# Kernel optimization log

Measured on AMD Instinct MI355X. Metric: run time of the kernel, lower is better.

The kernel has to match this reference:

```python
import jax, jax.numpy as jnp
import numpy as np

BATCH, L, OUT, DIM, VOCAB, K = 25, 11, 4, 2048, 32000, 1024


def setup_inputs() -> dict:
    key = jax.random.key(0)
    k1, k2, k3 = jax.random.split(key, 3)
    h = jax.random.normal(k1, (BATCH, L, OUT, DIM), dtype=jnp.float32)
    lm_head_weight = jax.random.normal(k2, (VOCAB, DIM), dtype=jnp.float32) * 0.02
    index = jax.random.randint(k3, (BATCH, L, K), 0, VOCAB, dtype=jnp.int64)
    return {"h": h, "lm_head_weight": lm_head_weight, "index": index}


def reference(h, lm_head_weight, index):
    # Faithful to torch: full-vocab matmul h @ weight.T, then gather selected ids.
    # h: (b, l, o, d); weight: (v, d) -> logits: (b, l, o, v)
    logits = jnp.einsum('blod,vd->blov', h, lm_head_weight)
    # gather along vocab dim with index (b, l, k) expanded over the o axis
    b, l, o, v = logits.shape
    idx = jnp.broadcast_to(index[:, :, None, :], (b, l, o, index.shape[-1]))
    result = jnp.take_along_axis(logits, idx, axis=3)  # (b, l, o, k)
    return result
```

## Files before the change

kernel.cpp:

```cpp
#include <hip/hip_runtime.h>

#define BATCH 25
#define LSEQ  11
#define OUTR  4
#define DIM   2048
#define VOCAB 32000
#define KSEL  1024

typedef _Float16 half8  __attribute__((ext_vector_type(8)));
typedef float    floatx4 __attribute__((ext_vector_type(4)));

#define WH_BYTES ((size_t)VOCAB * DIM * 2)

__global__ __launch_bounds__(256) void conv_f16(const float* __restrict__ w,
                                                _Float16* __restrict__ wh) {
    const size_t i = ((size_t)blockIdx.x * 256 + threadIdx.x) * 8;
    const floatx4 a = __builtin_nontemporal_load((const floatx4*)(w + i));
    const floatx4 b = __builtin_nontemporal_load((const floatx4*)(w + i + 4));
    half8 hv;
    hv[0] = (_Float16)a[0]; hv[1] = (_Float16)a[1];
    hv[2] = (_Float16)a[2]; hv[3] = (_Float16)a[3];
    hv[4] = (_Float16)b[0]; hv[5] = (_Float16)b[1];
    hv[6] = (_Float16)b[2]; hv[7] = (_Float16)b[3];
    *(half8*)(wh + i) = hv;
}

#define TPW 4
#define KPB (4 * TPW * 16)
#define NKC (KSEL / KPB)
#define ROWE 2080

__global__ __launch_bounds__(256) void gather_mfma(
    const float*    __restrict__ h,
    const _Float16* __restrict__ wh,
    const int*      __restrict__ index,
    float*          __restrict__ out)
{
    __shared__ _Float16 hs[OUTR * ROWE];

    const int bl   = blockIdx.x / NKC;
    const int kc   = blockIdx.x % NKC;
    const int tid  = threadIdx.x;
    const int wave = tid >> 6;
    const int lane = tid & 63;
    const int quad = lane >> 4;
    const int n    = lane & 15;
    const int row  = lane & 3;

    const float* hp = h + (size_t)bl * (OUTR * DIM);
#pragma unroll
    for (int o = 0; o < OUTR; ++o) {
        const int e = o * DIM + tid * 8;
        const floatx4 a = *(const floatx4*)(hp + e);
        const floatx4 b = *(const floatx4*)(hp + e + 4);
        half8 hv;
        hv[0] = (_Float16)a[0]; hv[1] = (_Float16)a[1];
        hv[2] = (_Float16)a[2]; hv[3] = (_Float16)a[3];
        hv[4] = (_Float16)b[0]; hv[5] = (_Float16)b[1];
        hv[6] = (_Float16)b[2]; hv[7] = (_Float16)b[3];
        *(half8*)(hs + o * ROWE + tid * 8) = hv;
    }
    __syncthreads();

    const int kb_blk = kc * KPB;
    const _Float16* bptr[TPW];
#pragma unroll
    for (int t = 0; t < TPW; ++t) {
        const int k_id = kb_blk + (wave * TPW + t) * 16 + n;
        const int ridx = index[(size_t)bl * KSEL + k_id];
        bptr[t] = wh + (size_t)ridx * DIM + quad * 8;
    }

    const _Float16* aptr = hs + row * ROWE + quad * 8;

    floatx4 acc[TPW];
#pragma unroll
    for (int t = 0; t < TPW; ++t) acc[t] = (floatx4){0.f, 0.f, 0.f, 0.f};

#pragma unroll 4
    for (int ks = 0; ks < DIM / 32; ++ks) {
        const half8 a = *(const half8*)(aptr + ks * 32);
        half8 b[TPW];
#pragma unroll
        for (int t = 0; t < TPW; ++t)
            b[t] = *(const half8*)(bptr[t] + ks * 32);
#pragma unroll
        for (int t = 0; t < TPW; ++t)
            acc[t] = __builtin_amdgcn_mfma_f32_16x16x32_f16(a, b[t], acc[t], 0, 0, 0);
    }

    if (quad == 0) {
        float* op = out + (size_t)bl * (OUTR * KSEL) + kb_blk;
#pragma unroll
        for (int t = 0; t < TPW; ++t) {
            const int kcol = (wave * TPW + t) * 16 + n;
#pragma unroll
            for (int r = 0; r < OUTR; ++r)
                op[r * KSEL + kcol] = acc[t][r];
        }
    }
}

#define FKPB 64
#define FKPW 16

__global__ __launch_bounds__(256) void ehead_f32_kernel(
    const float* __restrict__ h,
    const float* __restrict__ wt,
    const int*   __restrict__ index,
    float*       __restrict__ out)
{
    const int nkc = KSEL / FKPB;
    const int bl  = blockIdx.x / nkc;
    const int kc  = blockIdx.x % nkc;
    const int kbase = kc * FKPB;

    __shared__ float hsf[OUTR * DIM];
    const float* hp = h + (size_t)bl * (OUTR * DIM);
    const int tid = threadIdx.x;
#pragma unroll
    for (int i = 0; i < (OUTR * DIM) / (256 * 4); ++i) {
        const int e = (i * 256 + tid) * 4;
        *(float4*)&hsf[e] = *(const float4*)&hp[e];
    }
    __syncthreads();

    const int wave = tid >> 6;
    const int lane = tid & 63;
    const int* ip = index + (size_t)bl * KSEL + kbase + wave * FKPW;
    float*     op = out   + (size_t)bl * (OUTR * KSEL) + kbase + wave * FKPW;

    for (int g = 0; g < FKPW; g += 4) {
        const float4* r0 = (const float4*)(wt + (size_t)ip[g + 0] * DIM);
        const float4* r1 = (const float4*)(wt + (size_t)ip[g + 1] * DIM);
        const float4* r2 = (const float4*)(wt + (size_t)ip[g + 2] * DIM);
        const float4* r3 = (const float4*)(wt + (size_t)ip[g + 3] * DIM);
        float acc[OUTR][4];
#pragma unroll
        for (int o = 0; o < OUTR; ++o)
#pragma unroll
            for (int kk = 0; kk < 4; ++kk) acc[o][kk] = 0.f;
#pragma unroll
        for (int c = 0; c < DIM / 256; ++c) {
            const int off = c * 64 + lane;
            const float4 w0 = r0[off];
            const float4 w1 = r1[off];
            const float4 w2 = r2[off];
            const float4 w3 = r3[off];
#pragma unroll
            for (int o = 0; o < OUTR; ++o) {
                const float4 hv = *(const float4*)&hsf[o * DIM + off * 4];
                acc[o][0] += hv.x * w0.x + hv.y * w0.y + hv.z * w0.z + hv.w * w0.w;
                acc[o][1] += hv.x * w1.x + hv.y * w1.y + hv.z * w1.z + hv.w * w1.w;
                acc[o][2] += hv.x * w2.x + hv.y * w2.y + hv.z * w2.z + hv.w * w2.w;
                acc[o][3] += hv.x * w3.x + hv.y * w3.y + hv.z * w3.z + hv.w * w3.w;
            }
        }
#pragma unroll
        for (int o = 0; o < OUTR; ++o)
#pragma unroll
            for (int kk = 0; kk < 4; ++kk) {
                float v = acc[o][kk];
#pragma unroll
                for (int s = 32; s >= 1; s >>= 1) v += __shfl_xor(v, s, 64);
                acc[o][kk] = v;
            }
        if (lane < 16) {
            float v = 0.f;
#pragma unroll
            for (int oo = 0; oo < OUTR; ++oo)
#pragma unroll
                for (int qq = 0; qq < 4; ++qq)
                    v = (oo * 4 + qq == lane) ? acc[oo][qq] : v;
            op[(lane >> 2) * KSEL + g + (lane & 3)] = v;
        }
    }
}

extern "C" void kernel_launch(void* const* d_in, const int* in_sizes, int n_in,
                              void* d_out, int out_size, void* d_ws, size_t ws_size,
                              hipStream_t stream) {
    const float* h   = (const float*)d_in[0];
    const float* wt  = (const float*)d_in[1];
    const int*   idx = (const int*)d_in[2];
    float*       out = (float*)d_out;

    if (ws_size >= WH_BYTES) {
        _Float16* wh = (_Float16*)d_ws;
        conv_f16<<<(VOCAB * DIM) / (256 * 8), 256, 0, stream>>>(wt, wh);
        const int grid = BATCH * LSEQ * NKC;
        gather_mfma<<<grid, 256, 0, stream>>>(h, wh, idx, out);
    } else {
        const int grid = BATCH * LSEQ * (KSEL / FKPB);
        ehead_f32_kernel<<<grid, 256, 0, stream>>>(h, wt, idx, out);
    }
}
```

Before: 518.4 us.

## Replace gathered GEMV with full-vocab tiled MFMA GEMM then gather

Instead of converting the whole weight to fp16 and doing per-row gathered dot products, this converts only h to fp16 and pads it to 1152 rows. It then runs a 128x128 tiled MFMA GEMM against the fp32 weight, converting to fp16 inside the tile loads, and writes transposed fp16 logits to workspace. A final kernel gathers the selected vocab ids from those logits. This drops the full weight conversion pass and the scattered row gathers, at the cost of computing the full vocab (about 30x more FLOPs), storing the logits in fp16, and a GEMM with no double buffering.

```diff
diff --git a/kernel.cpp b/kernel.cpp
--- a/kernel.cpp
+++ b/kernel.cpp
@@ -7,98 +7,122 @@
 #define VOCAB 32000
 #define KSEL  1024
 
+#define MROWS (BATCH * LSEQ * OUTR)
+#define MPAD  1152
+#define MT 128
+#define NT 128
+#define BK 32
+#define LDT 36
+
 typedef _Float16 half8  __attribute__((ext_vector_type(8)));
+typedef _Float16 half4  __attribute__((ext_vector_type(4)));
 typedef float    floatx4 __attribute__((ext_vector_type(4)));
 
-#define WH_BYTES ((size_t)VOCAB * DIM * 2)
-
-__global__ __launch_bounds__(256) void conv_f16(const float* __restrict__ w,
-                                                _Float16* __restrict__ wh) {
+#define LOGITS_ELEMS ((size_t)VOCAB * MPAD)
+#define A_OFF        LOGITS_ELEMS
+#define WS_BYTES     ((LOGITS_ELEMS + (size_t)MPAD * DIM) * 2)
+
+__global__ __launch_bounds__(256) void conv_h(const float* __restrict__ h,
+                                              _Float16* __restrict__ A) {
     const size_t i = ((size_t)blockIdx.x * 256 + threadIdx.x) * 8;
-    const floatx4 a = __builtin_nontemporal_load((const floatx4*)(w + i));
-    const floatx4 b = __builtin_nontemporal_load((const floatx4*)(w + i + 4));
-    half8 hv;
-    hv[0] = (_Float16)a[0]; hv[1] = (_Float16)a[1];
-    hv[2] = (_Float16)a[2]; hv[3] = (_Float16)a[3];
-    hv[4] = (_Float16)b[0]; hv[5] = (_Float16)b[1];
-    hv[6] = (_Float16)b[2]; hv[7] = (_Float16)b[3];
-    *(half8*)(wh + i) = hv;
-}
-
-#define TPW 4
-#define KPB (4 * TPW * 16)
-#define NKC (KSEL / KPB)
-#define ROWE 2080
-
-__global__ __launch_bounds__(256) void gather_mfma(
-    const float*    __restrict__ h,
-    const _Float16* __restrict__ wh,
-    const int*      __restrict__ index,
-    float*          __restrict__ out)
-{
-    __shared__ _Float16 hs[OUTR * ROWE];
-
-    const int bl   = blockIdx.x / NKC;
-    const int kc   = blockIdx.x % NKC;
-    const int tid  = threadIdx.x;
-    const int wave = tid >> 6;
-    const int lane = tid & 63;
-    const int quad = lane >> 4;
-    const int n    = lane & 15;
-    const int row  = lane & 3;
-
-    const float* hp = h + (size_t)bl * (OUTR * DIM);
-#pragma unroll
-    for (int o = 0; o < OUTR; ++o) {
-        const int e = o * DIM + tid * 8;
-        const floatx4 a = *(const floatx4*)(hp + e);
-        const floatx4 b = *(const floatx4*)(hp + e + 4);
-        half8 hv;
+    const int row = (int)(i >> 11);
+    half8 hv = {};
+    if (row < MROWS) {
+        const floatx4 a = *(const floatx4*)(h + i);
+        const floatx4 b = *(const floatx4*)(h + i + 4);
         hv[0] = (_Float16)a[0]; hv[1] = (_Float16)a[1];
         hv[2] = (_Float16)a[2]; hv[3] = (_Float16)a[3];
         hv[4] = (_Float16)b[0]; hv[5] = (_Float16)b[1];
         hv[6] = (_Float16)b[2]; hv[7] = (_Float16)b[3];
-        *(half8*)(hs + o * ROWE + tid * 8) = hv;
-    }
-    __syncthreads();
-
-    const int kb_blk = kc * KPB;
-    const _Float16* bptr[TPW];
-#pragma unroll
-    for (int t = 0; t < TPW; ++t) {
-        const int k_id = kb_blk + (wave * TPW + t) * 16 + n;
-        const int ridx = index[(size_t)bl * KSEL + k_id];
-        bptr[t] = wh + (size_t)ridx * DIM + quad * 8;
-    }
-
-    const _Float16* aptr = hs + row * ROWE + quad * 8;
-
-    floatx4 acc[TPW];
-#pragma unroll
-    for (int t = 0; t < TPW; ++t) acc[t] = (floatx4){0.f, 0.f, 0.f, 0.f};
-
-#pragma unroll 4
-    for (int ks = 0; ks < DIM / 32; ++ks) {
-        const half8 a = *(const half8*)(aptr + ks * 32);
-        half8 b[TPW];
-#pragma unroll
-        for (int t = 0; t < TPW; ++t)
-            b[t] = *(const half8*)(bptr[t] + ks * 32);
-#pragma unroll
-        for (int t = 0; t < TPW; ++t)
-            acc[t] = __builtin_amdgcn_mfma_f32_16x16x32_f16(a, b[t], acc[t], 0, 0, 0);
-    }
-
-    if (quad == 0) {
-        float* op = out + (size_t)bl * (OUTR * KSEL) + kb_blk;
-#pragma unroll
-        for (int t = 0; t < TPW; ++t) {
-            const int kcol = (wave * TPW + t) * 16 + n;
-#pragma unroll
-            for (int r = 0; r < OUTR; ++r)
-                op[r * KSEL + kcol] = acc[t][r];
-        }
-    }
+    }
+    *(half8*)(A + i) = hv;
+}
+
+__global__ __launch_bounds__(256) void gemm_logits(
+    const _Float16* __restrict__ A,
+    const float*    __restrict__ W,
+    _Float16*       __restrict__ Ct)
+{
+    __shared__ _Float16 As[MT * LDT];
+    __shared__ _Float16 Bs[NT * LDT];
+
+    const int m0 = blockIdx.x * MT;
+    const int n0 = blockIdx.y * NT;
+    const int tid  = threadIdx.x;
+    const int wave = tid >> 6, lane = tid & 63;
+    const int quad = lane >> 4, l16 = lane & 15;
+    const int wm = (wave >> 1) * 64, wn = (wave & 1) * 64;
+
+    const int ar = tid >> 1, ac = (tid & 1) * 16;
+    const int bc = (tid & 7) * 4;
+
+    floatx4 acc[4][4];
+#pragma unroll
+    for (int mt = 0; mt < 4; ++mt)
+#pragma unroll
+        for (int nt = 0; nt < 4; ++nt) acc[mt][nt] = (floatx4){0.f, 0.f, 0.f, 0.f};
+
+    for (int k0 = 0; k0 < DIM; k0 += BK) {
+        __syncthreads();
+        {
+            const _Float16* src = A + (size_t)(m0 + ar) * DIM + k0 + ac;
+            *(half8*)(As + ar * LDT + ac)     = *(const half8*)src;
+            *(half8*)(As + ar * LDT + ac + 8) = *(const half8*)(src + 8);
+        }
+#pragma unroll
+        for (int i = 0; i < 4; ++i) {
+            const int r = i * 32 + (tid >> 3);
+            const floatx4 v = *(const floatx4*)(W + (size_t)(n0 + r) * DIM + k0 + bc);
+            half4 hv;
+            hv[0] = (_Float16)v[0]; hv[1] = (_Float16)v[1];
+            hv[2] = (_Float16)v[2]; hv[3] = (_Float16)v[3];
+            *(half4*)(Bs + r * LDT + bc) = hv;
+        }
+        __syncthreads();
+
+        half8 af[4], bf[4];
+#pragma unroll
+        for (int t = 0; t < 4; ++t) {
+            af[t] = *(const half8*)(As + (wm + t * 16 + l16) * LDT + quad * 8);
+            bf[t] = *(const half8*)(Bs + (wn + t * 16 + l16) * LDT + quad * 8);
+        }
+#pragma unroll
+        for (int mt = 0; mt < 4; ++mt)
+#pragma unroll
+            for (int nt = 0; nt < 4; ++nt)
+                acc[mt][nt] = __builtin_amdgcn_mfma_f32_16x16x32_f16(
+                    af[mt], bf[nt], acc[mt][nt], 0, 0, 0);
+    }
+
+#pragma unroll
+    for (int mt = 0; mt < 4; ++mt)
+#pragma unroll
+        for (int nt = 0; nt < 4; ++nt) {
+            const int m = m0 + wm + mt * 16 + quad * 4;
+            const int n = n0 + wn + nt * 16 + l16;
+            half4 hv;
+            hv[0] = (_Float16)acc[mt][nt][0];
+            hv[1] = (_Float16)acc[mt][nt][1];
+            hv[2] = (_Float16)acc[mt][nt][2];
+            hv[3] = (_Float16)acc[mt][nt][3];
+            *(half4*)(Ct + (size_t)n * MPAD + m) = hv;
+        }
+}
+
+__global__ __launch_bounds__(256) void gather_logits(
+    const _Float16* __restrict__ Ct,
+    const int*      __restrict__ index,
+    float*          __restrict__ out)
+{
+    const int gid = blockIdx.x * 256 + threadIdx.x;
+    const int bl = gid >> 10, k = gid & 1023;
+    const int ridx = index[gid];
+    const half4 v = *(const half4*)(Ct + (size_t)ridx * MPAD + bl * 4);
+    float* op = out + (size_t)bl * (OUTR * KSEL) + k;
+    op[0 * KSEL] = (float)v[0];
+    op[1 * KSEL] = (float)v[1];
+    op[2 * KSEL] = (float)v[2];
+    op[3 * KSEL] = (float)v[3];
 }
 
 #define FKPB 64
@@ -185,11 +209,16 @@
     const int*   idx = (const int*)d_in[2];
     float*       out = (float*)d_out;
 
-    if (ws_size >= WH_BYTES) {
-        _Float16* wh = (_Float16*)d_ws;
-        conv_f16<<<(VOCAB * DIM) / (256 * 8), 256, 0, stream>>>(wt, wh);
-        const int grid = BATCH * LSEQ * NKC;
-        gather_mfma<<<grid, 256, 0, stream>>>(h, wh, idx, out);
+    if (ws_size >= WS_BYTES) {
+        _Float16* Ct = (_Float16*)d_ws;
+        _Float16* A  = (_Float16*)d_ws + A_OFF;
+
+        conv_h<<<(MPAD * DIM) / (256 * 8), 256, 0, stream>>>(h, A);
+
+        dim3 grid(MPAD / MT, VOCAB / NT);
+        gemm_logits<<<grid, 256, 0, stream>>>(A, wt, Ct);
+
+        gather_logits<<<(BATCH * LSEQ * KSEL) / 256, 256, 0, stream>>>(Ct, idx, out);
     } else {
         const int grid = BATCH * LSEQ * (KSEL / FKPB);
         ehead_f32_kernel<<<grid, 256, 0, stream>>>(h, wt, idx, out);
```

Measured after the change: 629.0 us. +21.3%, slower.
